# Performance work log

Hardware: AMD Instinct MI355X
Metric: run time of the kernel (lower is better)

The kernel has to match this reference:

```python
import jax, jax.numpy as jnp
import numpy as np

N = 4096          # batch size
C = 256           # feature dim (out_dim)
N_DOMAINS = 8
LAST_RATIO = 0.7  # keep top last_ratio fraction of negatives per domain
TIME_WINDOW = 50
TEMP = 0.07


def _normalize(x):
    # F.normalize(x, dim=1): divide by max(||x||, eps)
    n = jnp.sqrt(jnp.sum(x * x, axis=1, keepdims=True))
    return x / jnp.maximum(n, 1e-12)


def setup_inputs() -> dict:
    key = jax.random.key(0)
    k1, k2, k3, k4 = jax.random.split(key, 4)
    return {
        "q": jax.random.normal(k1, (N, C), dtype=jnp.float32),
        "k": jax.random.normal(k2, (N, C), dtype=jnp.float32),
        "domain_label": jax.random.randint(k3, (N,), 0, N_DOMAINS, dtype=jnp.int32),
        "time_label": jax.random.randint(k4, (N,), 0, 200000, dtype=jnp.int32),
    }


def reference(q, k, domain_label, time_label):
    qn = _normalize(q)
    kn = _normalize(k)

    l_pos = jnp.sum(qn * kn, axis=1, keepdims=True)        # [N, 1]
    sims = jnp.einsum("nc,mc->nm", qn, kn)                 # [N, N] == q @ k.T
    l_neg = sims

    # --- per-domain hard-negative elimination (vectorized form of the torch loop) ---
    # For each row, within each domain's columns, rank negatives descending and
    # eliminate those with rank >= floor(count_d * last_ratio).
    counts = jnp.bincount(domain_label, length=N_DOMAINS)          # cols per domain
    prefix = jnp.cumsum(counts) - counts                            # exclusive prefix
    keep_thresh = jnp.floor(counts.astype(jnp.float32) * LAST_RATIO).astype(jnp.int32)

    # sort key: group by domain (ascending), value descending within domain.
    # similarities of unit vectors are in [-1, 1], so spacing domains by 4 is safe.
    sort_key = domain_label[None, :].astype(l_neg.dtype) * 4.0 - l_neg
    order = jnp.argsort(sort_key, axis=1)                           # [N, N] column ids
    dom_sorted = domain_label[order]                                # [N, N]
    rank_in_domain = jnp.arange(N, dtype=jnp.int32)[None, :] - prefix[dom_sorted]
    elim_sorted = rank_in_domain >= keep_thresh[dom_sorted]         # [N, N] bool
    rows = jnp.arange(N)[:, None]
    dom_mask = jnp.zeros((N, N), dtype=bool).at[rows, order].set(elim_sorted)

    # --- time-window masking: eliminate keys with |t_j - t_i| < window ---
    time_mask = jnp.abs(time_label[None, :] - time_label[:, None]) < TIME_WINDOW

    l_neg = jnp.where(dom_mask | time_mask, -jnp.inf, l_neg)

    logits = jnp.concatenate([l_pos, l_neg], axis=1) / TEMP         # [N, N+1]
    targets = jnp.zeros((N,), dtype=jnp.int32)
    feature = sims                                                  # unmasked q @ k.T
    return logits, targets, feature
```

## Files before the change

kernel.cpp:

```cpp
#include <hip/hip_runtime.h>
#include <math.h>

#define NROWS 4096
#define CDIM  256
#define NDOM  8
#define TWIN  50
#define KMAX  16

#define NEG_BIG -3.0e38f

typedef __attribute__((ext_vector_type(8))) short short8v;
typedef __attribute__((ext_vector_type(4))) float f32x4;

__device__ __forceinline__ unsigned f2key(float x) {
    unsigned b = __float_as_uint(x);
    return (b & 0x80000000u) ? ~b : (b | 0x80000000u);
}
__device__ __forceinline__ unsigned short f32_bf16(float f) {
    unsigned u = __float_as_uint(f);
    u += 0x7FFFu + ((u >> 16) & 1u);
    return (unsigned short)(u >> 16);
}
__device__ __forceinline__ float bf16_f32(unsigned short h) {
    return __uint_as_float(((unsigned)h) << 16);
}

__global__ __launch_bounds__(256) void normalize_kernel(
    const float* __restrict__ q, const float* __restrict__ k,
    unsigned short* __restrict__ qh, unsigned short* __restrict__ ql,
    unsigned short* __restrict__ kh, unsigned short* __restrict__ kl,
    float* __restrict__ lpos)
{
    const int wave = threadIdx.x >> 6, lane = threadIdx.x & 63;
    const int row = (blockIdx.x << 2) + wave;
    const size_t base = (size_t)row * CDIM + (lane << 2);
    float4 qv = *(const float4*)(q + base);
    float4 kv = *(const float4*)(k + base);

    float sq = qv.x*qv.x + qv.y*qv.y + qv.z*qv.z + qv.w*qv.w;
    float sk = kv.x*kv.x + kv.y*kv.y + kv.z*kv.z + kv.w*kv.w;
    #pragma unroll
    for (int s = 32; s > 0; s >>= 1) {
        sq += __shfl_xor(sq, s);
        sk += __shfl_xor(sk, s);
    }
    const float dq = fmaxf(sqrtf(sq), 1e-12f);
    const float dk = fmaxf(sqrtf(sk), 1e-12f);
    float qo[4] = { qv.x/dq, qv.y/dq, qv.z/dq, qv.w/dq };
    float ko[4] = { kv.x/dk, kv.y/dk, kv.z/dk, kv.w/dk };

    unsigned short qhb[4], qlb[4], khb[4], klb[4];
    #pragma unroll
    for (int i = 0; i < 4; ++i) {
        qhb[i] = f32_bf16(qo[i]); qlb[i] = f32_bf16(qo[i] - bf16_f32(qhb[i]));
        khb[i] = f32_bf16(ko[i]); klb[i] = f32_bf16(ko[i] - bf16_f32(khb[i]));
    }
    uint2 pk;
    pk.x = (unsigned)qhb[0] | ((unsigned)qhb[1] << 16);
    pk.y = (unsigned)qhb[2] | ((unsigned)qhb[3] << 16);
    *(uint2*)(qh + base) = pk;
    pk.x = (unsigned)qlb[0] | ((unsigned)qlb[1] << 16);
    pk.y = (unsigned)qlb[2] | ((unsigned)qlb[3] << 16);
    *(uint2*)(ql + base) = pk;
    pk.x = (unsigned)khb[0] | ((unsigned)khb[1] << 16);
    pk.y = (unsigned)khb[2] | ((unsigned)khb[3] << 16);
    *(uint2*)(kh + base) = pk;
    pk.x = (unsigned)klb[0] | ((unsigned)klb[1] << 16);
    pk.y = (unsigned)klb[2] | ((unsigned)klb[3] << 16);
    *(uint2*)(kl + base) = pk;

    float dp = qo[0]*ko[0] + qo[1]*ko[1] + qo[2]*ko[2] + qo[3]*ko[3];
    #pragma unroll
    for (int s = 32; s > 0; s >>= 1) dp += __shfl_xor(dp, s);
    if (lane == 0) lpos[row] = dp;
}

__global__ void domain_kernel(const int* __restrict__ dlab,
                              int* __restrict__ counts, int* __restrict__ prefix,
                              int* __restrict__ keep, int* __restrict__ cols)
{
    __shared__ int scnt[NDOM], spos[NDOM];
    const int tid = threadIdx.x;
    if (tid < NDOM) scnt[tid] = 0;
    __syncthreads();
    for (int j = tid; j < NROWS; j += blockDim.x) atomicAdd(&scnt[dlab[j]], 1);
    __syncthreads();
    if (tid == 0) {
        int acc = 0;
        for (int d = 0; d < NDOM; ++d) {
            const int c = scnt[d];
            counts[d] = c;
            prefix[d] = acc;
            spos[d]   = acc;
            keep[d]   = (int)floorf((float)c * 0.7f);
            acc += c;
        }
    }
    __syncthreads();
    for (int j = tid; j < NROWS; j += blockDim.x) {
        const int d = dlab[j];
        const int p = atomicAdd(&spos[d], 1);
        cols[p] = j;
    }
}

#define BM  128
#define BK  32
#define LDK 36
__global__ __launch_bounds__(256) void gemm_mfma_kernel(
    const unsigned short* __restrict__ qh, const unsigned short* __restrict__ ql,
    const unsigned short* __restrict__ kh, const unsigned short* __restrict__ kl,
    float* __restrict__ C)
{
    __shared__ unsigned short Ah[BM * LDK], Al[BM * LDK];
    __shared__ unsigned short Bh[BM * LDK], Bl[BM * LDK];

    const int t  = threadIdx.x;
    const int wv = t >> 6, l = t & 63;
    const int wr = wv >> 1, wc = wv & 1;
    const int bm = blockIdx.y * BM, bn = blockIdx.x * BM;

    f32x4 acc[4][4];
    #pragma unroll
    for (int i = 0; i < 4; ++i)
        #pragma unroll
        for (int j = 0; j < 4; ++j) acc[i][j] = (f32x4){0.f, 0.f, 0.f, 0.f};

    const int kg = (l >> 4) << 3;
    const int rl = l & 15;

    for (int k0 = 0; k0 < CDIM; k0 += BK) {
        __syncthreads();
        #pragma unroll
        for (int i = 0; i < 2; ++i) {
            const int c   = t + (i << 8);
            const int row = c >> 2, kq = (c & 3) << 3;
            const size_t ga = (size_t)(bm + row) * CDIM + k0 + kq;
            const size_t gb = (size_t)(bn + row) * CDIM + k0 + kq;
            const int la = row * LDK + kq;
            *(short8v*)&Ah[la] = *(const short8v*)&qh[ga];
            *(short8v*)&Al[la] = *(const short8v*)&ql[ga];
            *(short8v*)&Bh[la] = *(const short8v*)&kh[gb];
            *(short8v*)&Bl[la] = *(const short8v*)&kl[gb];
        }
        __syncthreads();

        short8v ah[4], al[4], bh[4], bl[4];
        #pragma unroll
        for (int f = 0; f < 4; ++f) {
            const int ar = (wr << 6) + (f << 4) + rl;
            const int br = (wc << 6) + (f << 4) + rl;
            ah[f] = *(const short8v*)&Ah[ar * LDK + kg];
            al[f] = *(const short8v*)&Al[ar * LDK + kg];
            bh[f] = *(const short8v*)&Bh[br * LDK + kg];
            bl[f] = *(const short8v*)&Bl[br * LDK + kg];
        }
        #pragma unroll
        for (int fr = 0; fr < 4; ++fr)
            #pragma unroll
            for (int fc = 0; fc < 4; ++fc) {
                acc[fr][fc] = __builtin_amdgcn_mfma_f32_16x16x32_bf16(ah[fr], bh[fc], acc[fr][fc], 0, 0, 0);
                acc[fr][fc] = __builtin_amdgcn_mfma_f32_16x16x32_bf16(al[fr], bh[fc], acc[fr][fc], 0, 0, 0);
                acc[fr][fc] = __builtin_amdgcn_mfma_f32_16x16x32_bf16(ah[fr], bl[fc], acc[fr][fc], 0, 0, 0);
            }
    }

    const int rq = (l >> 4) << 2;
    #pragma unroll
    for (int fr = 0; fr < 4; ++fr)
        #pragma unroll
        for (int fc = 0; fc < 4; ++fc) {
            const size_t mbase = (size_t)(bm + (wr << 6) + (fr << 4) + rq);
            const int    n     = bn + (wc << 6) + (fc << 4) + rl;
            #pragma unroll
            for (int r = 0; r < 4; ++r)
                C[(mbase + r) * NROWS + n] = acc[fr][fc][r];
        }
}

__global__ __launch_bounds__(512) void select_logits_kernel(
    const float* __restrict__ sims, const int* __restrict__ cols,
    const int* __restrict__ counts, const int* __restrict__ prefix,
    const int* __restrict__ keep, const int* __restrict__ dlab,
    const int* __restrict__ tlab, const float* __restrict__ lpos,
    float* __restrict__ logits, float* __restrict__ targets)
{
    __shared__ float srow[NROWS];
    __shared__ unsigned sthr[NDOM];

    const int row = blockIdx.x, tid = threadIdx.x;
    const float* g = sims + (size_t)row * NROWS;
    ((float4*)srow)[tid]       = ((const float4*)g)[tid];
    ((float4*)srow)[tid + 512] = ((const float4*)g)[tid + 512];
    __syncthreads();

    const int wave = tid >> 6, lane = tid & 63;
    const int cnt = counts[wave], off = prefix[wave], m = keep[wave];

    unsigned key[KMAX];
    #pragma unroll
    for (int tt = 0; tt < KMAX; ++tt) {
        const int idx = lane + (tt << 6);
        unsigned kk = 0u;
        if (idx < cnt) kk = f2key(srow[cols[off + idx]]);
        key[tt] = kk;
    }

    unsigned lo = 0u, hi = 0xFFFFFFFFu;
    for (int it = 0; it < 32; ++it) {
        const unsigned mid = lo + ((hi - lo) >> 1);
        int c = 0;
        #pragma unroll
        for (int tt = 0; tt < KMAX; ++tt)
            c += (int)__popcll(__ballot(key[tt] > mid));
        if (c > m) lo = mid + 1u; else hi = mid;
    }
    if (lane == 0) sthr[wave] = lo;
    __syncthreads();

    const int ti = tlab[row];
    float* orow = logits + (size_t)row * (NROWS + 1);
    if (tid == 0) {
        orow[0] = lpos[row] / 0.07f;
        targets[row] = 0.0f;
    }
    #pragma unroll
    for (int it = 0; it < 8; ++it) {
        const int j = tid + (it << 9);
        const float s = srow[j];
        const int   d = dlab[j];
        int dt = tlab[j] - ti; dt = dt < 0 ? -dt : dt;
        const bool kept = (f2key(s) > sthr[d]) && (dt >= TWIN);
        orow[1 + j] = kept ? s / 0.07f : NEG_BIG;
    }
}

extern "C" void kernel_launch(void* const* d_in, const int* in_sizes, int n_in,
                              void* d_out, int out_size, void* d_ws, size_t ws_size,
                              hipStream_t stream)
{
    const float* q    = (const float*)d_in[0];
    const float* k    = (const float*)d_in[1];
    const int*   dlab = (const int*)d_in[2];
    const int*   tlab = (const int*)d_in[3];

    float* out     = (float*)d_out;
    float* logits  = out;
    float* targets = out + (size_t)NROWS * (NROWS + 1);
    float* feature = targets + NROWS;

    unsigned short* qh = (unsigned short*)d_ws;
    unsigned short* ql = qh + (size_t)NROWS * CDIM;
    unsigned short* kh = ql + (size_t)NROWS * CDIM;
    unsigned short* kl = kh + (size_t)NROWS * CDIM;
    float*    lpos   = (float*)(kl + (size_t)NROWS * CDIM);
    int*      cols   = (int*)(lpos + NROWS);
    int*      counts = cols + NROWS;
    int*      prefix = counts + NDOM;
    int*      keep   = prefix + NDOM;

    normalize_kernel<<<NROWS / 4, 256, 0, stream>>>(q, k, qh, ql, kh, kl, lpos);
    domain_kernel<<<1, 512, 0, stream>>>(dlab, counts, prefix, keep, cols);
    gemm_mfma_kernel<<<dim3(NROWS / BM, NROWS / BM), 256, 0, stream>>>(qh, ql, kh, kl, feature);
    select_logits_kernel<<<NROWS, 512, 0, stream>>>(feature, cols, counts, prefix, keep,
                                                    dlab, tlab, lpos, logits, targets);
}
```

Before: 244.3 us.

## Replace 32-step bisection threshold search with 4-pass radix select in LDS

The per-domain threshold for hard-negative elimination was found by a 32-iteration binary search over the key space, each step doing 16 ballots. It now uses a radix select over 8-bit digits. Each level builds a 256-bin LDS histogram with atomics, runs a wave prefix scan to find the bin holding the target rank, and exits early once that bin has a single element. This cuts the number of passes over the keys, at the cost of LDS atomics, extra shared memory, and edge cases around ties and empty domains.

Result: faster. 220.8 us (-9.6%).

```diff
diff --git a/kernel.cpp b/kernel.cpp
--- a/kernel.cpp
+++ b/kernel.cpp
@@ -186,6 +186,7 @@
     float* __restrict__ logits, float* __restrict__ targets)
 {
     __shared__ float srow[NROWS];
+    __shared__ int hist[NDOM][256];
     __shared__ unsigned sthr[NDOM];
 
     const int row = blockIdx.x, tid = threadIdx.x;
@@ -196,6 +197,7 @@
 
     const int wave = tid >> 6, lane = tid & 63;
     const int cnt = counts[wave], off = prefix[wave], m = keep[wave];
+    int* h = hist[wave];
 
     unsigned key[KMAX];
     #pragma unroll
@@ -206,16 +208,62 @@
         key[tt] = kk;
     }
 
-    unsigned lo = 0u, hi = 0xFFFFFFFFu;
-    for (int it = 0; it < 32; ++it) {
-        const unsigned mid = lo + ((hi - lo) >> 1);
-        int c = 0;
-        #pragma unroll
-        for (int tt = 0; tt < KMAX; ++tt)
-            c += (int)__popcll(__ballot(key[tt] > mid));
-        if (c > m) lo = mid + 1u; else hi = mid;
-    }
-    if (lane == 0) sthr[wave] = lo;
+    unsigned thrkey = 0xFFFFFFFFu;
+    if (cnt > 0) {
+        unsigned pref = 0;
+        int r = m;
+        for (int lev = 3; lev >= 0; --lev) {
+            const int sh = lev << 3;
+            #pragma unroll
+            for (int i = 0; i < 4; ++i) h[lane + (i << 6)] = 0;
+            const unsigned hmask = (lev == 3) ? 0u : (0xFFFFFFFFu << (sh + 8));
+            #pragma unroll
+            for (int tt = 0; tt < KMAX; ++tt) {
+                const int idx = lane + (tt << 6);
+                if (idx < cnt && (key[tt] & hmask) == (pref & hmask))
+                    atomicAdd(&h[(key[tt] >> sh) & 255], 1);
+            }
+            int v[4];
+            #pragma unroll
+            for (int j = 0; j < 4; ++j) v[j] = h[255 - (lane << 2) - j];
+            const int lsum = v[0] + v[1] + v[2] + v[3];
+            int x = lsum;
+            #pragma unroll
+            for (int s = 1; s < 64; s <<= 1) {
+                const int y = __shfl_up(x, s);
+                if (lane >= s) x += y;
+            }
+            int ex = x - lsum;
+            int hit = -1, rn = 0, hv = 0;
+            #pragma unroll
+            for (int j = 0; j < 4; ++j) {
+                if (hit < 0 && r >= ex && r < ex + v[j]) {
+                    hit = 255 - (lane << 2) - j; rn = r - ex; hv = v[j];
+                }
+                ex += v[j];
+            }
+            const unsigned long long mk = __ballot(hit >= 0);
+            const int src = (int)__ffsll(mk) - 1;
+            const int bin  = __shfl(hit, src);
+            r              = __shfl(rn,  src);
+            const int binv = __shfl(hv,  src);
+            pref = (pref & ~(0xFFu << sh)) | (((unsigned)bin) << sh);
+            if (lev == 0) { thrkey = pref; break; }
+            if (binv == 1) {
+                const unsigned m2 = 0xFFFFFFFFu << sh;
+                unsigned mine = 0;
+                #pragma unroll
+                for (int tt = 0; tt < KMAX; ++tt) {
+                    const int idx = lane + (tt << 6);
+                    if (idx < cnt && (key[tt] & m2) == (pref & m2)) mine = key[tt];
+                }
+                const unsigned long long mk2 = __ballot(mine != 0u);
+                thrkey = __shfl(mine, (int)__ffsll(mk2) - 1);
+                break;
+            }
+        }
+    }
+    if (lane == 0) sthr[wave] = thrkey;
     __syncthreads();
 
     const int ti = tlab[row];
```
